# Kernel tuning notes

Hardware: AMD Instinct MI355X
Metric: run time of the kernel (lower is better)

The kernel has to match this reference:

```python
import jax, jax.numpy as jnp
import numpy as np

N = 131072          # events
N_OBS = 64          # observables
HID = [512, 512, 512]          # trunk hidden widths
SUB_HID = [512, 256]           # per-pair subnetwork hidden widths
P = 3                          # number of pairings


def _glorot(key, shape):
    fan_in, fan_out = shape[-2], shape[-1]
    lim = np.sqrt(6.0 / (fan_in + fan_out)).astype(np.float32)
    return jax.random.uniform(key, shape, jnp.float32, -lim, lim)


def setup_inputs() -> dict:
    key = jax.random.key(0)
    ks = jax.random.split(key, 16)
    x = jax.random.normal(ks[0], (N, N_OBS), jnp.float32)
    y = jax.random.randint(ks[1], (N,), 0, 3)
    pairs = jnp.array([[0, 1], [0, 2], [1, 2]], dtype=jnp.int32)
    # trunk params
    W0 = _glorot(ks[2], (N_OBS, HID[0])); b0 = jnp.zeros((HID[0],), jnp.float32)
    W1 = _glorot(ks[3], (HID[0], HID[1])); b1 = jnp.zeros((HID[1],), jnp.float32)
    W2 = _glorot(ks[4], (HID[1], HID[2])); b2 = jnp.zeros((HID[2],), jnp.float32)
    # stacked per-pair subnetwork params (all P subnets share shapes)
    SW0 = _glorot(ks[5], (P, HID[2], SUB_HID[0])); Sb0 = jnp.zeros((P, SUB_HID[0]), jnp.float32)
    SW1 = _glorot(ks[6], (P, SUB_HID[0], SUB_HID[1])); Sb1 = jnp.zeros((P, SUB_HID[1]), jnp.float32)
    SW2 = _glorot(ks[7], (P, SUB_HID[1], 1)); Sb2 = jnp.zeros((P, 1), jnp.float32)
    return {"x": x, "y": y, "pairs": pairs,
            "W0": W0, "b0": b0, "W1": W1, "b1": b1, "W2": W2, "b2": b2,
            "SW0": SW0, "Sb0": Sb0, "SW1": SW1, "Sb1": Sb1, "SW2": SW2, "Sb2": Sb2}


def reference(x, y, pairs, W0, b0, W1, b1, W2, b2, SW0, Sb0, SW1, Sb1, SW2, Sb2):
    relu = jax.nn.relu
    # Trunk. Note: in the torch module with dropout_prob>0, the first Linear sits at
    # layer index 1, so the activation is applied to the raw input as well (eval-mode
    # dropout == identity). We reproduce that exactly.
    h = relu(x) @ W0 + b0
    h = relu(h) @ W1 + b1
    repr_ = relu(h) @ W2 + b2                      # [N, HID[-1]]

    # Per-pair membership masks (jit-safe stand-in for the variable-size gather):
    # mask[p, n] = True iff y[n] is one of the two labels of pairing p.
    mask = (y[None, :] == pairs[:, 0:1]) | (y[None, :] == pairs[:, 1:2])  # [P, N] bool

    # Per-pair RatioModel subnetworks, batched over the pair dim.
    # Same activation-before-every-Linear pattern as the trunk (dropout indices).
    hs = jnp.einsum('nd,pdh->pnh', relu(repr_), SW0) + Sb0[:, None, :]
    hs = jnp.einsum('pnh,phk->pnk', relu(hs), SW1) + Sb1[:, None, :]
    logit = jnp.einsum('pnk,pko->pno', relu(hs), SW2) + Sb2[:, None, :]  # [P, N, 1]
    s_hat = jnp.clip(jax.nn.sigmoid(logit[..., 0]), 1e-9, None)          # [P, N]
    r_hat = (1.0 - s_hat) / s_hat                                        # [P, N]

    maskf = mask.astype(s_hat.dtype)
    return repr_, r_hat * maskf, s_hat * maskf, mask
```

## Files before the change

kernel.cpp:

```cpp
#include <hip/hip_runtime.h>
#include <hip/hip_bf16.h>
#include <stdint.h>

#define NE 131072
#define CHUNK 32768

typedef __attribute__((ext_vector_type(8))) short bf16x8;
typedef __attribute__((ext_vector_type(4))) float f32x4;

__device__ __forceinline__ unsigned short f2bf(float f) {
  unsigned u = __float_as_uint(f);
  u += 0x7FFF + ((u >> 16) & 1);
  return (unsigned short)(u >> 16);
}
__device__ __forceinline__ float bf2f(unsigned short h) {
  return __uint_as_float((unsigned)h << 16);
}

__device__ __forceinline__ void gload_lds16(const void* g, void* l) {
  __builtin_amdgcn_global_load_lds(
      (const __attribute__((address_space(1))) unsigned*)g,
      (__attribute__((address_space(3))) unsigned*)l, 16, 0, 0);
}

__global__ void transpose_cvt(const float* __restrict__ src,
                              unsigned short* __restrict__ dst,
                              int K, int Nc) {
  int p = blockIdx.y;
  long base = (long)p * K * Nc;
  int tot = K * Nc;
  for (int i = blockIdx.x * blockDim.x + threadIdx.x; i < tot;
       i += gridDim.x * blockDim.x) {
    int n = i / K, k = i - n * K;
    dst[base + i] = f2bf(src[base + (long)k * Nc + n]);
  }
}

__global__ void relu_cvt_x(const float4* __restrict__ x,
                           ushort4* __restrict__ xb) {
  int i = blockIdx.x * blockDim.x + threadIdx.x;
  float4 v = x[i];
  ushort4 o;
  o.x = f2bf(fmaxf(v.x, 0.f));
  o.y = f2bf(fmaxf(v.y, 0.f));
  o.z = f2bf(fmaxf(v.z, 0.f));
  o.w = f2bf(fmaxf(v.w, 0.f));
  xb[i] = o;
}

__global__ __launch_bounds__(256, 2) void gemm_bf16(
    const unsigned short* __restrict__ A, long aZ,
    const unsigned short* __restrict__ Bt, long bZ,
    const float* __restrict__ bias, long biasZ,
    float* __restrict__ outF,
    unsigned short* __restrict__ outA, long cZ,
    int K, int Nc) {
  __shared__ unsigned short As[128 * 32];
  __shared__ unsigned short Bs[128 * 32];
  const int z = blockIdx.z;
  A += (long)z * aZ;
  Bt += (long)z * bZ;
  bias += (long)z * biasZ;
  if (outF) outF += (long)z * cZ;
  if (outA) outA += (long)z * cZ;

  const int tid = threadIdx.x;
  const int wave = tid >> 6, lane = tid & 63;
  const int wr = wave >> 1, wc = wave & 1;
  const int lr = lane & 15, lh = lane >> 4;
  const long row0 = (long)blockIdx.x * 128;
  const int col0 = blockIdx.y * 128;

  f32x4 acc[4][4];
#pragma unroll
  for (int m = 0; m < 4; ++m)
#pragma unroll
    for (int n = 0; n < 4; ++n) acc[m][n] = (f32x4){0.f, 0.f, 0.f, 0.f};

  const int nk = K >> 5;
  for (int kt = 0; kt < nk; ++kt) {
    const int k0 = kt << 5;
#pragma unroll
    for (int i = 0; i < 2; ++i) {
      int c = i * 256 + wave * 64 + lane;
      int r = c >> 2, k8 = (c & 3) * 8;
      gload_lds16(A + (row0 + r) * K + k0 + k8, &As[(i * 256 + wave * 64) * 8]);
      gload_lds16(Bt + (long)(col0 + r) * K + k0 + k8,
                  &Bs[(i * 256 + wave * 64) * 8]);
    }
    __syncthreads();
    bf16x8 af[4], bfr[4];
#pragma unroll
    for (int m = 0; m < 4; ++m)
      af[m] = *(const bf16x8*)&As[(wr * 64 + m * 16 + lr) * 32 + lh * 8];
#pragma unroll
    for (int n = 0; n < 4; ++n)
      bfr[n] = *(const bf16x8*)&Bs[(wc * 64 + n * 16 + lr) * 32 + lh * 8];
#pragma unroll
    for (int m = 0; m < 4; ++m)
#pragma unroll
      for (int n = 0; n < 4; ++n)
        acc[m][n] =
            __builtin_amdgcn_mfma_f32_16x16x32_bf16(af[m], bfr[n], acc[m][n], 0, 0, 0);
    __syncthreads();
  }

  float bv[4];
#pragma unroll
  for (int n = 0; n < 4; ++n) bv[n] = bias[col0 + wc * 64 + n * 16 + lr];
#pragma unroll
  for (int m = 0; m < 4; ++m) {
    long rbase = row0 + wr * 64 + m * 16 + lh * 4;
#pragma unroll
    for (int r = 0; r < 4; ++r) {
      long rr = rbase + r;
#pragma unroll
      for (int n = 0; n < 4; ++n) {
        int cc = col0 + wc * 64 + n * 16 + lr;
        float v = acc[m][n][r] + bv[n];
        if (outF) outF[rr * Nc + cc] = v;
        if (outA) outA[rr * Nc + cc] = f2bf(fmaxf(v, 0.f));
      }
    }
  }
}

__global__ __launch_bounds__(512) void gemm_sw1_head(
    const unsigned short* __restrict__ A3,
    const unsigned short* __restrict__ SW1t,
    const float* __restrict__ Sb1,
    const unsigned short* __restrict__ W2b,
    const float* __restrict__ Sb2,
    const int* __restrict__ y,
    const int* __restrict__ pairs,
    int r0,
    float* __restrict__ outR, float* __restrict__ outS,
    float* __restrict__ outM) {
  __shared__ unsigned short As[128 * 32];
  __shared__ unsigned short Bs[256 * 32];
  __shared__ float part[4][128];

  const int p = blockIdx.z;
  const unsigned short* A = A3 + (long)p * CHUNK * 512;
  const unsigned short* Bt = SW1t + (long)p * 256 * 512;
  const float* bias = Sb1 + p * 256;
  const unsigned short* w2 = W2b + p * 256;

  const int tid = threadIdx.x;
  const int wave = tid >> 6, lane = tid & 63;
  const int wr = wave >> 2, wc = wave & 3;
  const int lr = lane & 15, lh = lane >> 4;
  const long row0 = (long)blockIdx.x * 128;

  f32x4 acc[4][4];
#pragma unroll
  for (int m = 0; m < 4; ++m)
#pragma unroll
    for (int n = 0; n < 4; ++n) acc[m][n] = (f32x4){0.f, 0.f, 0.f, 0.f};

  for (int kt = 0; kt < 16; ++kt) {
    const int k0 = kt << 5;
    gload_lds16(A + (row0 + (tid >> 2)) * 512 + k0 + (tid & 3) * 8,
                &As[wave * 64 * 8]);
#pragma unroll
    for (int i = 0; i < 2; ++i) {
      int c = i * 512 + tid;
      int r = c >> 2, k8 = (c & 3) * 8;
      gload_lds16(Bt + (long)r * 512 + k0 + k8, &Bs[(i * 512 + wave * 64) * 8]);
    }
    __syncthreads();
    bf16x8 af[4], bfr[4];
#pragma unroll
    for (int m = 0; m < 4; ++m)
      af[m] = *(const bf16x8*)&As[(wr * 64 + m * 16 + lr) * 32 + lh * 8];
#pragma unroll
    for (int n = 0; n < 4; ++n)
      bfr[n] = *(const bf16x8*)&Bs[(wc * 64 + n * 16 + lr) * 32 + lh * 8];
#pragma unroll
    for (int m = 0; m < 4; ++m)
#pragma unroll
      for (int n = 0; n < 4; ++n)
        acc[m][n] =
            __builtin_amdgcn_mfma_f32_16x16x32_bf16(af[m], bfr[n], acc[m][n], 0, 0, 0);
    __syncthreads();
  }

  float bv[4], w2v[4];
#pragma unroll
  for (int n = 0; n < 4; ++n) {
    int cc = wc * 64 + n * 16 + lr;
    bv[n] = bias[cc];
    w2v[n] = bf2f(w2[cc]);
  }
#pragma unroll
  for (int m = 0; m < 4; ++m) {
#pragma unroll
    for (int r = 0; r < 4; ++r) {
      float s = 0.f;
#pragma unroll
      for (int n = 0; n < 4; ++n) {
        float v = fmaxf(acc[m][n][r] + bv[n], 0.f);
        s += v * w2v[n];
      }
#pragma unroll
      for (int off = 1; off < 16; off <<= 1) s += __shfl_xor(s, off);
      if (lr == 0) part[wc][wr * 64 + m * 16 + lh * 4 + r] = s;
    }
  }
  __syncthreads();
  if (tid < 128) {
    float logit = part[0][tid] + part[1][tid] + part[2][tid] + part[3][tid] +
                  Sb2[p];
    float s = 1.f / (1.f + expf(-logit));
    s = fmaxf(s, 1e-9f);
    float r = (1.f - s) / s;
    long n = (long)r0 + row0 + tid;
    int yv = y[n];
    float mf = (yv == pairs[p * 2] || yv == pairs[p * 2 + 1]) ? 1.f : 0.f;
    outR[(long)p * NE + n] = r * mf;
    outS[(long)p * NE + n] = s * mf;
    outM[(long)p * NE + n] = mf;
  }
}

extern "C" void kernel_launch(void* const* d_in, const int* in_sizes, int n_in,
                              void* d_out, int out_size, void* d_ws, size_t ws_size,
                              hipStream_t stream) {
  const float* x   = (const float*)d_in[0];
  const int*   y   = (const int*)d_in[1];
  const int*   prs = (const int*)d_in[2];
  const float* W0  = (const float*)d_in[3];
  const float* b0  = (const float*)d_in[4];
  const float* W1  = (const float*)d_in[5];
  const float* b1  = (const float*)d_in[6];
  const float* W2  = (const float*)d_in[7];
  const float* b2  = (const float*)d_in[8];
  const float* SW0 = (const float*)d_in[9];
  const float* Sb0 = (const float*)d_in[10];
  const float* SW1 = (const float*)d_in[11];
  const float* Sb1 = (const float*)d_in[12];
  const float* SW2 = (const float*)d_in[13];
  const float* Sb2 = (const float*)d_in[14];

  uint8_t* ws = (uint8_t*)d_ws;
  size_t off = 0;
  auto take = [&](size_t bytes) -> void* {
    void* ptr = ws + off;
    off = (off + bytes + 255) & ~(size_t)255;
    return ptr;
  };
  unsigned short* W0t  = (unsigned short*)take((size_t)64 * 512 * 2);
  unsigned short* W1t  = (unsigned short*)take((size_t)512 * 512 * 2);
  unsigned short* W2t  = (unsigned short*)take((size_t)512 * 512 * 2);
  unsigned short* SW0t = (unsigned short*)take((size_t)3 * 512 * 512 * 2);
  unsigned short* SW1t = (unsigned short*)take((size_t)3 * 256 * 512 * 2);
  unsigned short* SW2b = (unsigned short*)take((size_t)3 * 256 * 2);
  unsigned short* Xb   = (unsigned short*)take((size_t)NE * 64 * 2);
  unsigned short* A3   = (unsigned short*)take((size_t)3 * CHUNK * 512 * 2);
  unsigned short* T0   = A3;
  unsigned short* T1   = A3 + (size_t)CHUNK * 512;
  unsigned short* bufR = (unsigned short*)take((size_t)CHUNK * 512 * 2);

  float* out   = (float*)d_out;
  float* outRe = out;
  float* outR  = out + (size_t)NE * 512;
  float* outS  = outR + (size_t)3 * NE;
  float* outM  = outS + (size_t)3 * NE;

  transpose_cvt<<<dim3(128, 1), 256, 0, stream>>>(W0, W0t, 64, 512);
  transpose_cvt<<<dim3(1024, 1), 256, 0, stream>>>(W1, W1t, 512, 512);
  transpose_cvt<<<dim3(1024, 1), 256, 0, stream>>>(W2, W2t, 512, 512);
  transpose_cvt<<<dim3(1024, 3), 256, 0, stream>>>(SW0, SW0t, 512, 512);
  transpose_cvt<<<dim3(512, 3), 256, 0, stream>>>(SW1, SW1t, 512, 256);
  transpose_cvt<<<dim3(1, 3), 256, 0, stream>>>(SW2, SW2b, 256, 1);
  relu_cvt_x<<<dim3(NE * 64 / 4 / 256), 256, 0, stream>>>((const float4*)x,
                                                          (ushort4*)Xb);

  for (int c = 0; c < NE / CHUNK; ++c) {
    size_t r0 = (size_t)c * CHUNK;
    gemm_bf16<<<dim3(CHUNK / 128, 4, 1), 256, 0, stream>>>(
        Xb + r0 * 64, 0, W0t, 0, b0, 0, nullptr, T0, 0, 64, 512);
    gemm_bf16<<<dim3(CHUNK / 128, 4, 1), 256, 0, stream>>>(
        T0, 0, W1t, 0, b1, 0, nullptr, T1, 0, 512, 512);
    gemm_bf16<<<dim3(CHUNK / 128, 4, 1), 256, 0, stream>>>(
        T1, 0, W2t, 0, b2, 0, outRe + r0 * 512, bufR, 0, 512, 512);
    gemm_bf16<<<dim3(CHUNK / 128, 4, 3), 256, 0, stream>>>(
        bufR, 0, SW0t, (long)512 * 512, Sb0, 512, nullptr, A3,
        (long)CHUNK * 512, 512, 512);
    gemm_sw1_head<<<dim3(CHUNK / 128, 1, 3), 512, 0, stream>>>(
        A3, SW1t, Sb1, SW2b, Sb2, y, prs, (int)r0, outR, outS, outM);
  }
}
```

Baseline: 767.0 us.

## Fuse subnet SW0/SW1/head GEMMs in LDS, widen trunk tiles, enlarge chunks

```diff
diff --git a/kernel.cpp b/kernel.cpp
--- a/kernel.cpp
+++ b/kernel.cpp
@@ -3,7 +3,6 @@
 #include <stdint.h>
 
 #define NE 131072
-#define CHUNK 32768
 
 typedef __attribute__((ext_vector_type(8))) short bf16x8;
 typedef __attribute__((ext_vector_type(4))) float f32x4;
@@ -23,16 +22,35 @@
       (__attribute__((address_space(3))) unsigned*)l, 16, 0, 0);
 }
 
-__global__ void transpose_cvt(const float* __restrict__ src,
-                              unsigned short* __restrict__ dst,
-                              int K, int Nc) {
-  int p = blockIdx.y;
-  long base = (long)p * K * Nc;
-  int tot = K * Nc;
-  for (int i = blockIdx.x * blockDim.x + threadIdx.x; i < tot;
-       i += gridDim.x * blockDim.x) {
-    int n = i / K, k = i - n * K;
-    dst[base + i] = f2bf(src[base + (long)k * Nc + n]);
+__global__ void weight_prep(const float* __restrict__ W0, const float* __restrict__ W1,
+                            const float* __restrict__ W2, const float* __restrict__ SW0,
+                            const float* __restrict__ SW1, const float* __restrict__ SW2,
+                            unsigned short* W0t, unsigned short* W1t,
+                            unsigned short* W2t, unsigned short* SW0t,
+                            unsigned short* SW1t, unsigned short* SW2b) {
+  __shared__ float tile[32][33];
+  const int u = blockIdx.y;
+  const float* src; unsigned short* dst; int K, Nc;
+  if (u == 0)      { src = W0;  dst = W0t;  K = 64;  Nc = 512; }
+  else if (u == 1) { src = W1;  dst = W1t;  K = 512; Nc = 512; }
+  else if (u == 2) { src = W2;  dst = W2t;  K = 512; Nc = 512; }
+  else if (u < 6)  { int p = u - 3; src = SW0 + (long)p * 512 * 512; dst = SW0t + (long)p * 512 * 512; K = 512; Nc = 512; }
+  else if (u < 9)  { int p = u - 6; src = SW1 + (long)p * 512 * 256; dst = SW1t + (long)p * 256 * 512; K = 512; Nc = 256; }
+  else             { int p = u - 9; src = SW2 + (long)p * 256;       dst = SW2b + (long)p * 256;       K = 256; Nc = 1; }
+  const int tkn = K >> 5;
+  const int tk = blockIdx.x % tkn, tn = blockIdx.x / tkn;
+  if (tn >= ((Nc + 31) >> 5)) return;
+  const int k0 = tk * 32, n0 = tn * 32;
+  const int tx = threadIdx.x & 31, ty = threadIdx.x >> 5;
+  if (n0 + tx < Nc)
+#pragma unroll
+    for (int j = 0; j < 4; ++j)
+      tile[ty * 4 + j][tx] = src[(long)(k0 + ty * 4 + j) * Nc + n0 + tx];
+  __syncthreads();
+#pragma unroll
+  for (int j = 0; j < 4; ++j) {
+    int n = n0 + ty * 4 + j;
+    if (n < Nc) dst[(long)n * K + k0 + tx] = f2bf(tile[tx][ty * 4 + j]);
   }
 }
 
@@ -48,149 +66,192 @@
   xb[i] = o;
 }
 
-__global__ __launch_bounds__(256, 2) void gemm_bf16(
-    const unsigned short* __restrict__ A, long aZ,
-    const unsigned short* __restrict__ Bt, long bZ,
-    const float* __restrict__ bias, long biasZ,
+__global__ __launch_bounds__(512) void gemmW(
+    const unsigned short* __restrict__ A,
+    const unsigned short* __restrict__ Bt,
+    const float* __restrict__ bias,
     float* __restrict__ outF,
-    unsigned short* __restrict__ outA, long cZ,
-    int K, int Nc) {
+    unsigned short* __restrict__ outA,
+    int K) {
   __shared__ unsigned short As[128 * 32];
-  __shared__ unsigned short Bs[128 * 32];
-  const int z = blockIdx.z;
-  A += (long)z * aZ;
-  Bt += (long)z * bZ;
-  bias += (long)z * biasZ;
-  if (outF) outF += (long)z * cZ;
-  if (outA) outA += (long)z * cZ;
-
+  __shared__ unsigned short Bs[512 * 32];
   const int tid = threadIdx.x;
   const int wave = tid >> 6, lane = tid & 63;
-  const int wr = wave >> 1, wc = wave & 1;
+  const int wm = wave >> 2, wn = wave & 3;
   const int lr = lane & 15, lh = lane >> 4;
   const long row0 = (long)blockIdx.x * 128;
-  const int col0 = blockIdx.y * 128;
-
-  f32x4 acc[4][4];
+
+  f32x4 acc[4][8];
 #pragma unroll
   for (int m = 0; m < 4; ++m)
 #pragma unroll
-    for (int n = 0; n < 4; ++n) acc[m][n] = (f32x4){0.f, 0.f, 0.f, 0.f};
+    for (int n = 0; n < 8; ++n) acc[m][n] = (f32x4){0.f, 0.f, 0.f, 0.f};
 
   const int nk = K >> 5;
   for (int kt = 0; kt < nk; ++kt) {
     const int k0 = kt << 5;
-#pragma unroll
-    for (int i = 0; i < 2; ++i) {
-      int c = i * 256 + wave * 64 + lane;
-      int r = c >> 2, k8 = (c & 3) * 8;
-      gload_lds16(A + (row0 + r) * K + k0 + k8, &As[(i * 256 + wave * 64) * 8]);
-      gload_lds16(Bt + (long)(col0 + r) * K + k0 + k8,
-                  &Bs[(i * 256 + wave * 64) * 8]);
+    gload_lds16(A + (row0 + (tid >> 2)) * K + k0 + (tid & 3) * 8,
+                &As[wave * 64 * 8]);
+#pragma unroll
+    for (int i = 0; i < 4; ++i) {
+      int c = i * 512 + tid;
+      gload_lds16(Bt + (long)(c >> 2) * K + k0 + (c & 3) * 8,
+                  &Bs[(i * 512 + wave * 64) * 8]);
     }
     __syncthreads();
-    bf16x8 af[4], bfr[4];
+    bf16x8 a[4], b[8];
 #pragma unroll
     for (int m = 0; m < 4; ++m)
-      af[m] = *(const bf16x8*)&As[(wr * 64 + m * 16 + lr) * 32 + lh * 8];
-#pragma unroll
-    for (int n = 0; n < 4; ++n)
-      bfr[n] = *(const bf16x8*)&Bs[(wc * 64 + n * 16 + lr) * 32 + lh * 8];
+      a[m] = *(const bf16x8*)&As[(wm * 64 + m * 16 + lr) * 32 + lh * 8];
+#pragma unroll
+    for (int n = 0; n < 8; ++n)
+      b[n] = *(const bf16x8*)&Bs[(wn * 128 + n * 16 + lr) * 32 + lh * 8];
 #pragma unroll
     for (int m = 0; m < 4; ++m)
 #pragma unroll
-      for (int n = 0; n < 4; ++n)
+      for (int n = 0; n < 8; ++n)
         acc[m][n] =
-            __builtin_amdgcn_mfma_f32_16x16x32_bf16(af[m], bfr[n], acc[m][n], 0, 0, 0);
+            __builtin_amdgcn_mfma_f32_16x16x32_bf16(a[m], b[n], acc[m][n], 0, 0, 0);
     __syncthreads();
   }
 
-  float bv[4];
-#pragma unroll
-  for (int n = 0; n < 4; ++n) bv[n] = bias[col0 + wc * 64 + n * 16 + lr];
+  float bv[8];
+#pragma unroll
+  for (int n = 0; n < 8; ++n) bv[n] = bias[wn * 128 + n * 16 + lr];
 #pragma unroll
   for (int m = 0; m < 4; ++m) {
-    long rbase = row0 + wr * 64 + m * 16 + lh * 4;
 #pragma unroll
     for (int r = 0; r < 4; ++r) {
-      long rr = rbase + r;
-#pragma unroll
-      for (int n = 0; n < 4; ++n) {
-        int cc = col0 + wc * 64 + n * 16 + lr;
+      long e = row0 + wm * 64 + m * 16 + lh * 4 + r;
+#pragma unroll
+      for (int n = 0; n < 8; ++n) {
+        int oc = wn * 128 + n * 16 + lr;
         float v = acc[m][n][r] + bv[n];
-        if (outF) outF[rr * Nc + cc] = v;
-        if (outA) outA[rr * Nc + cc] = f2bf(fmaxf(v, 0.f));
+        if (outF) outF[e * 512 + oc] = v;
+        if (outA) outA[e * 512 + oc] = f2bf(fmaxf(v, 0.f));
       }
     }
   }
 }
 
-__global__ __launch_bounds__(512) void gemm_sw1_head(
-    const unsigned short* __restrict__ A3,
+__global__ __launch_bounds__(512) void subnet_fused(
+    const unsigned short* __restrict__ bufR,
+    const unsigned short* __restrict__ SW0t,
+    const float* __restrict__ Sb0,
     const unsigned short* __restrict__ SW1t,
     const float* __restrict__ Sb1,
     const unsigned short* __restrict__ W2b,
     const float* __restrict__ Sb2,
-    const int* __restrict__ y,
-    const int* __restrict__ pairs,
+    const int* __restrict__ y, const int* __restrict__ pairs,
     int r0,
     float* __restrict__ outR, float* __restrict__ outS,
     float* __restrict__ outM) {
-  __shared__ unsigned short As[128 * 32];
-  __shared__ unsigned short Bs[256 * 32];
+  __shared__ unsigned short h0[65536];
+  __shared__ float lbias[512];
   __shared__ float part[4][128];
-
   const int p = blockIdx.z;
-  const unsigned short* A = A3 + (long)p * CHUNK * 512;
-  const unsigned short* Bt = SW1t + (long)p * 256 * 512;
-  const float* bias = Sb1 + p * 256;
-  const unsigned short* w2 = W2b + p * 256;
-
-  const int tid = threadIdx.x;
-  const int wave = tid >> 6, lane = tid & 63;
-  const int wr = wave >> 2, wc = wave & 3;
+  const int tid = threadIdx.x, wave = tid >> 6, lane = tid & 63;
   const int lr = lane & 15, lh = lane >> 4;
-  const long row0 = (long)blockIdx.x * 128;
-
-  f32x4 acc[4][4];
-#pragma unroll
-  for (int m = 0; m < 4; ++m)
+  const long erow0 = (long)blockIdx.x * 128;
+  const unsigned short* Wt = SW0t + (long)p * 512 * 512;
+  const unsigned short* Rb = bufR + erow0 * 512;
+
+  lbias[tid] = Sb0[p * 512 + tid];
+
+  const int wm4 = wave >> 1, wn2 = wave & 1;
+  f32x4 acc[8][4];
+#pragma unroll
+  for (int m = 0; m < 8; ++m)
 #pragma unroll
     for (int n = 0; n < 4; ++n) acc[m][n] = (f32x4){0.f, 0.f, 0.f, 0.f};
+
+  unsigned short* Ast = h0;
+  unsigned short* Bst = h0 + 16384;
 
   for (int kt = 0; kt < 16; ++kt) {
     const int k0 = kt << 5;
-    gload_lds16(A + (row0 + (tid >> 2)) * 512 + k0 + (tid & 3) * 8,
-                &As[wave * 64 * 8]);
-#pragma unroll
-    for (int i = 0; i < 2; ++i) {
+#pragma unroll
+    for (int i = 0; i < 4; ++i) {
       int c = i * 512 + tid;
-      int r = c >> 2, k8 = (c & 3) * 8;
-      gload_lds16(Bt + (long)r * 512 + k0 + k8, &Bs[(i * 512 + wave * 64) * 8]);
-    }
+      gload_lds16(Wt + (long)(c >> 2) * 512 + k0 + (c & 3) * 8,
+                  &Ast[(i * 512 + wave * 64) * 8]);
+    }
+    gload_lds16(Rb + (long)(tid >> 2) * 512 + k0 + (tid & 3) * 8,
+                &Bst[wave * 64 * 8]);
     __syncthreads();
-    bf16x8 af[4], bfr[4];
-#pragma unroll
-    for (int m = 0; m < 4; ++m)
-      af[m] = *(const bf16x8*)&As[(wr * 64 + m * 16 + lr) * 32 + lh * 8];
+    bf16x8 a[8], b[4];
+#pragma unroll
+    for (int m = 0; m < 8; ++m)
+      a[m] = *(const bf16x8*)&Ast[(wm4 * 128 + m * 16 + lr) * 32 + lh * 8];
 #pragma unroll
     for (int n = 0; n < 4; ++n)
-      bfr[n] = *(const bf16x8*)&Bs[(wc * 64 + n * 16 + lr) * 32 + lh * 8];
-#pragma unroll
-    for (int m = 0; m < 4; ++m)
+      b[n] = *(const bf16x8*)&Bst[(wn2 * 64 + n * 16 + lr) * 32 + lh * 8];
+#pragma unroll
+    for (int m = 0; m < 8; ++m)
 #pragma unroll
       for (int n = 0; n < 4; ++n)
         acc[m][n] =
-            __builtin_amdgcn_mfma_f32_16x16x32_bf16(af[m], bfr[n], acc[m][n], 0, 0, 0);
+            __builtin_amdgcn_mfma_f32_16x16x32_bf16(a[m], b[n], acc[m][n], 0, 0, 0);
     __syncthreads();
   }
 
-  float bv[4], w2v[4];
+#pragma unroll
+  for (int m = 0; m < 8; ++m) {
+    const int h4 = wm4 * 128 + m * 16 + lh * 4;
+    const f32x4 bv = *(const f32x4*)&lbias[h4];
+#pragma unroll
+    for (int n = 0; n < 4; ++n) {
+      const int e = wn2 * 64 + n * 16 + lr;
+      uint2 v;
+      unsigned short p0 = f2bf(fmaxf(acc[m][n][0] + bv[0], 0.f));
+      unsigned short p1 = f2bf(fmaxf(acc[m][n][1] + bv[1], 0.f));
+      unsigned short p2 = f2bf(fmaxf(acc[m][n][2] + bv[2], 0.f));
+      unsigned short p3 = f2bf(fmaxf(acc[m][n][3] + bv[3], 0.f));
+      v.x = (unsigned)p0 | ((unsigned)p1 << 16);
+      v.y = (unsigned)p2 | ((unsigned)p3 << 16);
+      const int byte = (e * 1024 + h4 * 2) ^ ((e & 7) << 4);
+      *reinterpret_cast<uint2*>(reinterpret_cast<char*>(h0) + byte) = v;
+    }
+  }
+  __syncthreads();
+
+  const int wm2 = wave >> 2, wn4 = wave & 3;
+  const unsigned short* W1p = SW1t + (long)p * 256 * 512;
+  f32x4 acc2[4][4];
+#pragma unroll
+  for (int m = 0; m < 4; ++m)
+#pragma unroll
+    for (int n = 0; n < 4; ++n) acc2[m][n] = (f32x4){0.f, 0.f, 0.f, 0.f};
+
+  for (int kt = 0; kt < 16; ++kt) {
+    const int k = kt * 32 + lh * 8;
+    bf16x8 a2[4], b2[4];
+#pragma unroll
+    for (int m = 0; m < 4; ++m) {
+      const int e = wm2 * 64 + m * 16 + lr;
+      const int byte = (e * 1024 + k * 2) ^ ((e & 7) << 4);
+      a2[m] = *reinterpret_cast<const bf16x8*>(
+          reinterpret_cast<const char*>(h0) + byte);
+    }
+#pragma unroll
+    for (int n = 0; n < 4; ++n) {
+      const int oc = wn4 * 64 + n * 16 + lr;
+      b2[n] = *(const bf16x8*)&W1p[(long)oc * 512 + k];
+    }
+#pragma unroll
+    for (int m = 0; m < 4; ++m)
+#pragma unroll
+      for (int n = 0; n < 4; ++n)
+        acc2[m][n] =
+            __builtin_amdgcn_mfma_f32_16x16x32_bf16(a2[m], b2[n], acc2[m][n], 0, 0, 0);
+  }
+
+  float b1v[4], w2v[4];
 #pragma unroll
   for (int n = 0; n < 4; ++n) {
-    int cc = wc * 64 + n * 16 + lr;
-    bv[n] = bias[cc];
-    w2v[n] = bf2f(w2[cc]);
+    const int oc = wn4 * 64 + n * 16 + lr;
+    b1v[n] = Sb1[p * 256 + oc];
+    w2v[n] = bf2f(W2b[p * 256 + oc]);
   }
 #pragma unroll
   for (int m = 0; m < 4; ++m) {
@@ -198,13 +259,11 @@
     for (int r = 0; r < 4; ++r) {
       float s = 0.f;
 #pragma unroll
-      for (int n = 0; n < 4; ++n) {
-        float v = fmaxf(acc[m][n][r] + bv[n], 0.f);
-        s += v * w2v[n];
-      }
+      for (int n = 0; n < 4; ++n)
+        s += fmaxf(acc2[m][n][r] + b1v[n], 0.f) * w2v[n];
 #pragma unroll
       for (int off = 1; off < 16; off <<= 1) s += __shfl_xor(s, off);
-      if (lr == 0) part[wc][wr * 64 + m * 16 + lh * 4 + r] = s;
+      if (lr == 0) part[wn4][wm2 * 64 + m * 16 + lh * 4 + r] = s;
     }
   }
   __syncthreads();
@@ -213,11 +272,11 @@
                   Sb2[p];
     float s = 1.f / (1.f + expf(-logit));
     s = fmaxf(s, 1e-9f);
-    float r = (1.f - s) / s;
-    long n = (long)r0 + row0 + tid;
+    float rr = (1.f - s) / s;
+    long n = r0 + erow0 + tid;
     int yv = y[n];
     float mf = (yv == pairs[p * 2] || yv == pairs[p * 2 + 1]) ? 1.f : 0.f;
-    outR[(long)p * NE + n] = r * mf;
+    outR[(long)p * NE + n] = rr * mf;
     outS[(long)p * NE + n] = s * mf;
     outM[(long)p * NE + n] = mf;
   }
@@ -256,10 +315,15 @@
   unsigned short* SW1t = (unsigned short*)take((size_t)3 * 256 * 512 * 2);
   unsigned short* SW2b = (unsigned short*)take((size_t)3 * 256 * 2);
   unsigned short* Xb   = (unsigned short*)take((size_t)NE * 64 * 2);
-  unsigned short* A3   = (unsigned short*)take((size_t)3 * CHUNK * 512 * 2);
-  unsigned short* T0   = A3;
-  unsigned short* T1   = A3 + (size_t)CHUNK * 512;
-  unsigned short* bufR = (unsigned short*)take((size_t)CHUNK * 512 * 2);
+  size_t fixed = off;
+
+  int chunk = 32768;
+  if (ws_size >= fixed + (size_t)2 * 131072 * 1024 + 4096) chunk = 131072;
+  else if (ws_size >= fixed + (size_t)2 * 65536 * 1024 + 4096) chunk = 65536;
+
+  unsigned short* T0 = (unsigned short*)take((size_t)chunk * 512 * 2);
+  unsigned short* T1 = (unsigned short*)take((size_t)chunk * 512 * 2);
+  unsigned short* bufR = T0;
 
   float* out   = (float*)d_out;
   float* outRe = out;
@@ -267,27 +331,18 @@
   float* outS  = outR + (size_t)3 * NE;
   float* outM  = outS + (size_t)3 * NE;
 
-  transpose_cvt<<<dim3(128, 1), 256, 0, stream>>>(W0, W0t, 64, 512);
-  transpose_cvt<<<dim3(1024, 1), 256, 0, stream>>>(W1, W1t, 512, 512);
-  transpose_cvt<<<dim3(1024, 1), 256, 0, stream>>>(W2, W2t, 512, 512);
-  transpose_cvt<<<dim3(1024, 3), 256, 0, stream>>>(SW0, SW0t, 512, 512);
-  transpose_cvt<<<dim3(512, 3), 256, 0, stream>>>(SW1, SW1t, 512, 256);
-  transpose_cvt<<<dim3(1, 3), 256, 0, stream>>>(SW2, SW2b, 256, 1);
+  weight_prep<<<dim3(256, 12), 256, 0, stream>>>(W0, W1, W2, SW0, SW1, SW2,
+                                                 W0t, W1t, W2t, SW0t, SW1t, SW2b);
   relu_cvt_x<<<dim3(NE * 64 / 4 / 256), 256, 0, stream>>>((const float4*)x,
                                                           (ushort4*)Xb);
 
-  for (int c = 0; c < NE / CHUNK; ++c) {
-    size_t r0 = (size_t)c * CHUNK;
-    gemm_bf16<<<dim3(CHUNK / 128, 4, 1), 256, 0, stream>>>(
-        Xb + r0 * 64, 0, W0t, 0, b0, 0, nullptr, T0, 0, 64, 512);
-    gemm_bf16<<<dim3(CHUNK / 128, 4, 1), 256, 0, stream>>>(
-        T0, 0, W1t, 0, b1, 0, nullptr, T1, 0, 512, 512);
-    gemm_bf16<<<dim3(CHUNK / 128, 4, 1), 256, 0, stream>>>(
-        T1, 0, W2t, 0, b2, 0, outRe + r0 * 512, bufR, 0, 512, 512);
-    gemm_bf16<<<dim3(CHUNK / 128, 4, 3), 256, 0, stream>>>(
-        bufR, 0, SW0t, (long)512 * 512, Sb0, 512, nullptr, A3,
-        (long)CHUNK * 512, 512, 512);
-    gemm_sw1_head<<<dim3(CHUNK / 128, 1, 3), 512, 0, stream>>>(
-        A3, SW1t, Sb1, SW2b, Sb2, y, prs, (int)r0, outR, outS, outM);
-  }
-}
+  for (int r0 = 0; r0 < NE; r0 += chunk) {
+    gemmW<<<dim3(chunk / 128), 512, 0, stream>>>(
+        Xb + (size_t)r0 * 64, W0t, b0, nullptr, T0, 64);
+    gemmW<<<dim3(chunk / 128), 512, 0, stream>>>(T0, W1t, b1, nullptr, T1, 512);
+    gemmW<<<dim3(chunk / 128), 512, 0, stream>>>(
+        T1, W2t, b2, outRe + (size_t)r0 * 512, bufR, 512);
+    subnet_fused<<<dim3(chunk / 128, 1, 3), 512, 0, stream>>>(
+        bufR, SW0t, Sb0, SW1t, Sb1, SW2b, Sb2, y, prs, r0, outR, outS, outM);
+  }
+}
```

Measured after the change: 856.4 us. 1.12x slower.
